# Kernel optimization log

Measured on AMD Instinct MI355X. Metric: run time of the kernel, lower is better.

The kernel has to match this reference:

```python
import jax, jax.numpy as jnp
import numpy as np

B, S, H = 2, 2048, 2048
NUM_HEADS, NUM_KV_HEADS, HEAD_DIM = 8, 1, 256
ROPE_THETA = 10000.0
NEG_INF = -1e9


def _rope_tables(seq_len, head_dim, base=ROPE_THETA):
    # cos/sin of shape [seq_len, head_dim], matching GemmaRotaryEmbedding
    inv_freq = 1.0 / (base ** (jnp.arange(0, head_dim, 2, dtype=jnp.float32) / head_dim))
    pos = jnp.arange(seq_len, dtype=jnp.float32)
    freqs = pos[:, None] * inv_freq[None, :]          # [S, D/2]
    emb = jnp.concatenate([freqs, freqs], axis=-1)    # [S, D]
    return jnp.cos(emb), jnp.sin(emb)


def _rotate_half(x):
    d = x.shape[-1] // 2
    return jnp.concatenate([-x[..., d:], x[..., :d]], axis=-1)


def setup_inputs() -> dict:
    key = jax.random.key(0)
    ks = jax.random.split(key, 5)
    hidden_states = jax.random.normal(ks[0], (B, S, H), dtype=jnp.float32)
    # additive causal mask: 0 where allowed, -inf above diagonal
    causal = jnp.tril(jnp.ones((S, S), dtype=bool))
    attention_mask = jnp.where(causal, 0.0, NEG_INF).astype(jnp.float32)[None, None]  # [1,1,S,S]
    sc = 1.0 / np.sqrt(H)
    Wq = jax.random.normal(ks[1], (H, NUM_HEADS * HEAD_DIM), dtype=jnp.float32) * sc
    Wk = jax.random.normal(ks[2], (H, NUM_KV_HEADS * HEAD_DIM), dtype=jnp.float32) * sc
    Wv = jax.random.normal(ks[3], (H, NUM_KV_HEADS * HEAD_DIM), dtype=jnp.float32) * sc
    Wo = jax.random.normal(ks[4], (NUM_HEADS * HEAD_DIM, H), dtype=jnp.float32) * sc
    return {"hidden_states": hidden_states, "attention_mask": attention_mask,
            "Wq": Wq, "Wk": Wk, "Wv": Wv, "Wo": Wo}


def reference(hidden_states, attention_mask, Wq, Wk, Wv, Wo):
    b, s, _ = hidden_states.shape
    g = NUM_HEADS // NUM_KV_HEADS  # query heads per kv head

    q = (hidden_states @ Wq).reshape(b, s, NUM_HEADS, HEAD_DIM).transpose(0, 2, 1, 3)      # [b,h,s,d]
    k = (hidden_states @ Wk).reshape(b, s, NUM_KV_HEADS, HEAD_DIM).transpose(0, 2, 1, 3)   # [b,kh,s,d]
    v = (hidden_states @ Wv).reshape(b, s, NUM_KV_HEADS, HEAD_DIM).transpose(0, 2, 1, 3)   # [b,kh,s,d]

    cos, sin = _rope_tables(s, HEAD_DIM)  # [s,d]
    cos = cos[None, None]                 # [1,1,s,d]
    sin = sin[None, None]
    q = q * cos + _rotate_half(q) * sin
    k = k * cos + _rotate_half(k) * sin

    # GQA attention without materializing repeated K/V: group query heads per kv head
    qg = q.reshape(b, NUM_KV_HEADS, g, s, HEAD_DIM)                       # [b,kh,g,s,d]
    scale = 1.0 / np.sqrt(HEAD_DIM)
    scores = jnp.einsum('bkgsd,bktd->bkgst', qg, k) * scale               # [b,kh,g,s,t]
    scores = scores + attention_mask[:, :, None]                          # broadcast [1,1,1,s,t]
    probs = jax.nn.softmax(scores, axis=-1)
    out = jnp.einsum('bkgst,bktd->bkgsd', probs, v)                       # [b,kh,g,s,d]
    out = out.reshape(b, NUM_HEADS, s, HEAD_DIM).transpose(0, 2, 1, 3).reshape(b, s, NUM_HEADS * HEAD_DIM)
    return out @ Wo
```

## Files before the change

kernel.cpp:

```cpp
#include <hip/hip_runtime.h>
#include <hip/hip_bf16.h>

typedef unsigned short u16;
typedef short short8 __attribute__((ext_vector_type(8)));
typedef float f32x4 __attribute__((ext_vector_type(4)));
typedef float f32x16 __attribute__((ext_vector_type(16)));
typedef u16 u16x4 __attribute__((ext_vector_type(4)));

__device__ __forceinline__ u16 f2bf(float f) {
    unsigned int u = __float_as_uint(f);
    u += 0x7fffu + ((u >> 16) & 1u);
    return (u16)(u >> 16);
}
__device__ __forceinline__ float bf2f(u16 s) {
    return __uint_as_float(((unsigned int)s) << 16);
}
__device__ __forceinline__ unsigned pack2(float lo, float hi) {
    union { __hip_bfloat162 h; unsigned u; } cv;
    cv.h = __float22bfloat162_rn(make_float2(lo, hi));
    return cv.u;
}
__device__ __forceinline__ f32x4 mfma16(short8 a, short8 b, f32x4 c) {
    return __builtin_amdgcn_mfma_f32_16x16x32_bf16(a, b, c, 0, 0, 0);
}
__device__ __forceinline__ f32x16 mfma32(short8 a, short8 b, f32x16 c) {
    return __builtin_amdgcn_mfma_f32_32x32x16_bf16(a, b, c, 0, 0, 0);
}
__device__ __forceinline__ void gld16(const void* g, void* l) {
    __builtin_amdgcn_global_load_lds(
        (const __attribute__((address_space(1))) unsigned int*)g,
        (__attribute__((address_space(3))) unsigned int*)l, 16, 0, 0);
}

#define BATCH 2
#define SEQ   2048
#define HID   2048
#define NH    8
#define HD    256
#define MROWS (BATCH * SEQ)

__global__ void k_cvt(const float* __restrict__ src, u16* __restrict__ dst, int n) {
    int i = (blockIdx.x * 256 + threadIdx.x) * 4;
    if (i >= n) return;
    float4 v = *(const float4*)(src + i);
    u16x4 o; o.x = f2bf(v.x); o.y = f2bf(v.y); o.z = f2bf(v.z); o.w = f2bf(v.w);
    *(u16x4*)(dst + i) = o;
}

__global__ __launch_bounds__(256) void k_wtall(const float* __restrict__ Wq,
                                               const float* __restrict__ Wk,
                                               const float* __restrict__ Wv,
                                               const float* __restrict__ Wo,
                                               u16* __restrict__ Wqkvt,
                                               u16* __restrict__ Wot) {
    const int cx = blockIdx.x;
    const float* W; u16* Wt; int N, n0;
    if (cx < 32)      { W = Wq; Wt = Wqkvt;                          N = 2048; n0 = cx << 6; }
    else if (cx < 36) { W = Wk; Wt = Wqkvt + (size_t)2048 * 2048;    N = 256;  n0 = (cx - 32) << 6; }
    else if (cx < 40) { W = Wv; Wt = Wqkvt + (size_t)2304 * 2048;    N = 256;  n0 = (cx - 36) << 6; }
    else              { W = Wo; Wt = Wot;                            N = 2048; n0 = (cx - 40) << 6; }

    __shared__ float tile[64][65];
    const int k0 = blockIdx.y << 6;
    const int tr = threadIdx.x >> 6, tc = threadIdx.x & 63;
#pragma unroll
    for (int i = 0; i < 16; i++)
        tile[i * 4 + tr][tc] = W[(size_t)(k0 + i * 4 + tr) * N + n0 + tc];
    __syncthreads();
#pragma unroll
    for (int i = 0; i < 16; i++) {
        int r = i * 4 + tr;
        Wt[(size_t)(n0 + r) * 2048 + k0 + tc] = f2bf(tile[tc][r]);
    }
}

__global__ __launch_bounds__(256) void k_vt(const u16* __restrict__ KVb, char* __restrict__ VS) {
    __shared__ u16 sT[64][72];
    const int bid = blockIdx.x;
    const int b = bid >> 7, kvt = (bid >> 2) & 31, dc = bid & 3;
    const int tr = threadIdx.x >> 6, tc = threadIdx.x & 63;
#pragma unroll
    for (int i = 0; i < 16; i++) {
        int kv = i * 4 + tr;
        sT[kv][tc] = KVb[((size_t)(b * SEQ + kvt * 64 + kv) << 9) + 256 + (dc << 6) + tc];
    }
    __syncthreads();
    char* obase = VS + ((size_t)b << 20) + (size_t)kvt * 32768;
#pragma unroll
    for (int e = 0; e < 2; e++) {
        int u = threadIdx.x * 2 + e;
        int dl = u >> 3, kvc = u & 7;
        union { u16 h[8]; uint4 q; } pk;
#pragma unroll
        for (int j = 0; j < 8; j++) pk.h[j] = sT[kvc * 8 + j][dl];
        int byte = dl * 512 + ((((dc << 7) + (kvc << 4))) ^ ((dl & 31) << 4));
        *(uint4*)(obase + byte) = pk.q;
    }
}

template<int FUSEQKV>
__global__ __launch_bounds__(256) void k_gemm(const u16* __restrict__ A,
                                              const u16* __restrict__ Bt,
                                              u16* __restrict__ Cq,
                                              u16* __restrict__ Ckv,
                                              float* __restrict__ Cf,
                                              int K, int nbx) {
    const int cpx = gridDim.x >> 3;
    const int t8  = (blockIdx.x & 7) * cpx + (blockIdx.x >> 3);
    const int m0 = (t8 / nbx) << 7;
    const int n0 = (t8 % nbx) << 7;

    const int tid = threadIdx.x, lane = tid & 63, wave = tid >> 6;
    const int g = lane >> 4, c = lane & 15;
    const int wrow = (wave >> 1) << 6, wcol = (wave & 1) << 6;

    __shared__ __align__(16) u16 sA[128 * 64];
    __shared__ __align__(16) u16 sB[128 * 64];

    const int srow = lane >> 3;
    const int scol = ((lane & 7) ^ srow) << 3;
    const u16* gA = A  + (size_t)(m0 + wave * 32 + srow) * K + scol;
    const u16* gB = Bt + (size_t)(n0 + wave * 32 + srow) * K + scol;
    u16* const lA = sA + wave * 32 * 64;
    u16* const lB = sB + wave * 32 * 64;

    f32x4 acc[4][4] = {};

    for (int k0 = 0; k0 < K; k0 += 64) {
        __syncthreads();
#pragma unroll
        for (int i = 0; i < 4; i++) {
            gld16(gA + k0 + (size_t)i * 8 * K, lA + i * 8 * 64);
            gld16(gB + k0 + (size_t)i * 8 * K, lB + i * 8 * 64);
        }
        __syncthreads();
#pragma unroll
        for (int ks = 0; ks < 2; ks++) {
            short8 aF[4], bF[4];
#pragma unroll
            for (int tt = 0; tt < 4; tt++) {
                const int ar = wrow + tt * 16 + c;
                const int br = wcol + tt * 16 + c;
                const int coff = ks * 64 + g * 16;
                aF[tt] = *(const short8*)((const char*)sA + ar * 128 + (coff ^ ((ar & 7) << 4)));
                bF[tt] = *(const short8*)((const char*)sB + br * 128 + (coff ^ ((br & 7) << 4)));
            }
#pragma unroll
            for (int mt = 0; mt < 4; mt++)
#pragma unroll
                for (int ntc = 0; ntc < 4; ntc++)
                    acc[mt][ntc] = mfma16(aF[mt], bF[ntc], acc[mt][ntc]);
        }
    }

#pragma unroll
    for (int mt = 0; mt < 4; mt++)
#pragma unroll
        for (int ntc = 0; ntc < 4; ntc++)
#pragma unroll
            for (int r = 0; r < 4; r++) {
                int row = m0 + wrow + mt * 16 + g * 4 + r;
                int col = n0 + wcol + ntc * 16 + c;
                float v = acc[mt][ntc][r];
                if (FUSEQKV) {
                    if (col < 2048) Cq [(size_t)row * 2048 + col] = f2bf(v);
                    else            Ckv[(size_t)row * 512 + (col - 2048)] = f2bf(v);
                } else {
                    Cf[(size_t)row * 2048 + col] = v;
                }
            }
}

__global__ void k_rope(u16* __restrict__ Qb, const u16* __restrict__ KVb,
                       char* __restrict__ KS) {
    int idx = blockIdx.x * 256 + threadIdx.x;
    const int QG = MROWS * NH * 16;
    if (idx < QG) {
        int row  = idx >> 7;
        int rest = idx & 127;
        int h = rest >> 4, d0 = (rest & 15) << 3;
        u16* base = Qb + (size_t)row * HID + h * HD + d0;
        int pos = row & (SEQ - 1);
        short8 lo = *(const short8*)(base);
        short8 hi = *(const short8*)(base + 128);
        short8 olo, ohi;
#pragma unroll
        for (int j = 0; j < 8; j++) {
            int d = d0 + j;
            float invf = __expf(-(float)d * (9.2103403719761836f / 128.0f));
            float ang = (float)pos * invf;
            float sn, cs; __sincosf(ang, &sn, &cs);
            float x0 = bf2f((u16)lo[j]);
            float x1 = bf2f((u16)hi[j]);
            olo[j] = (short)f2bf(x0 * cs - x1 * sn);
            ohi[j] = (short)f2bf(x1 * cs + x0 * sn);
        }
        *(short8*)(base)       = olo;
        *(short8*)(base + 128) = ohi;
    } else {
        int j0 = idx - QG;
        int row = j0 >> 4, d0 = (j0 & 15) << 3;
        const u16* src = KVb + (size_t)row * 512 + d0;
        int pos = row & (SEQ - 1);
        short8 lo = *(const short8*)(src);
        short8 hi = *(const short8*)(src + 128);
        short8 olo, ohi;
#pragma unroll
        for (int j = 0; j < 8; j++) {
            int d = d0 + j;
            float invf = __expf(-(float)d * (9.2103403719761836f / 128.0f));
            float ang = (float)pos * invf;
            float sn, cs; __sincosf(ang, &sn, &cs);
            float x0 = bf2f((u16)lo[j]);
            float x1 = bf2f((u16)hi[j]);
            olo[j] = (short)f2bf(x0 * cs - x1 * sn);
            ohi[j] = (short)f2bf(x1 * cs + x0 * sn);
        }
        int bb = row >> 11, sr = row & 2047;
        char* obase = KS + ((size_t)bb << 20) + (size_t)(sr >> 6) * 32768 + (sr & 63) * 512;
        int xr = (sr & 31) << 4;
        *(short8*)(obase + (((d0 << 1))       ^ xr)) = olo;
        *(short8*)(obase + (((d0 << 1) + 256) ^ xr)) = ohi;
    }
}

__global__ __launch_bounds__(256, 2) void k_attn(const u16* __restrict__ Q,
                                                 const char* __restrict__ KS,
                                                 const char* __restrict__ VS,
                                                 u16* __restrict__ Oa) {
    const int tid  = threadIdx.x;
    const int lane = tid & 63;
    const int wave = tid >> 6;
    const int l31  = lane & 31;
    const int hv   = lane >> 5;

    const int bid   = blockIdx.x;
    const int bh    = bid & 15;
    const int qpair = (bid >> 4) & 15;
    const int qidx  = (bid >> 8) ? (31 - qpair) : qpair;
    const int qb    = qidx << 6;
    const int b = bh >> 3, head = bh & 7;

    __shared__ __align__(16) char smem[66560];
    char*  const pK  = smem;
    char*  const pV  = smem + 32768;
    float* const sML = (float*)(smem + 65536);

    const int qg = qb + ((wave >> 1) << 5) + l31;
    short8 qf[16];
    {
        const u16* qptr = Q + (size_t)(b * SEQ + qg) * HID + head * HD + (hv << 3);
#pragma unroll
        for (int ks = 0; ks < 16; ks++)
            qf[ks] = *(const short8*)(qptr + (ks << 4));
    }

    f32x16 o[8] = {};
    float m = -1e30f, l = 0.f;

    const char* kgb = KS + ((size_t)b << 20);
    const char* vgb = VS + ((size_t)b << 20);
    const int   kxor  = l31 << 4;
    const char* kbase = pK + (((wave & 1) << 5) + l31) * 512;

    const int nt = qidx + 1;
    for (int t = 0; t < nt; t++) {
        __syncthreads();
#pragma unroll
        for (int i = 0; i < 8; i++) {
            int chunk = (i << 2) + wave;
            gld16(kgb + (size_t)t * 32768 + chunk * 1024 + lane * 16, pK + chunk * 1024);
            gld16(vgb + (size_t)t * 32768 + chunk * 1024 + lane * 16, pV + chunk * 1024);
        }
        __syncthreads();

        f32x16 sv0 = {}, sv1 = {};
#pragma unroll
        for (int ks = 0; ks < 16; ks += 2) {
            short8 kf0 = *(const short8*)(kbase + (((ks << 5) + (hv << 4)) ^ kxor));
            short8 kf1 = *(const short8*)(kbase + ((((ks + 1) << 5) + (hv << 4)) ^ kxor));
            sv0 = mfma32(kf0, qf[ks], sv0);
            sv1 = mfma32(kf1, qf[ks + 1], sv1);
        }
        f32x16 s = sv0 + sv1;

        float v[16];
        float mx = -3.0e38f;
        const bool diag = (t == nt - 1);
#pragma unroll
        for (int r = 0; r < 16; r++) {
            float x = s[r] * 0.0625f;
            if (diag) {
                int kvg = (t << 6) + ((wave & 1) << 5) + (r & 3) + ((r >> 2) << 3) + (hv << 2);
                if (kvg > qg) x = -3.0e38f;
            }
            v[r] = x;
            mx = fmaxf(mx, x);
        }
        mx = fmaxf(mx, __shfl_xor(mx, 32));
        if (!__all(mx <= m + 8.0f)) {
            float mn = fmaxf(m, mx);
            float sc = __expf(m - mn);
            l *= sc;
#pragma unroll
            for (int r = 0; r < 16; r++) {
                float scr = __shfl(sc, (r & 3) + ((r >> 2) << 3) + (hv << 2));
#pragma unroll
                for (int dt = 0; dt < 8; dt++) o[dt][r] *= scr;
            }
            m = mn;
        }
        float rs = 0.f;
#pragma unroll
        for (int r = 0; r < 16; r++) { v[r] = __expf(v[r] - m); rs += v[r]; }
        rs += __shfl_xor(rs, 32);
        l += rs;

        unsigned wd[8], pw[8];
#pragma unroll
        for (int i = 0; i < 8; i++) wd[i] = pack2(v[2 * i], v[2 * i + 1]);
#pragma unroll
        for (int i = 0; i < 8; i++) pw[i] = (unsigned)__shfl_xor((int)wd[i], 32);

#pragma unroll
        for (int ks2 = 0; ks2 < 2; ks2++) {
            union { unsigned u[4]; short8 s8; } fr;
            const int o4 = ks2 << 2;
            fr.u[0] = hv ? pw[o4 + 2] : wd[o4 + 0];
            fr.u[1] = hv ? pw[o4 + 3] : wd[o4 + 1];
            fr.u[2] = hv ? wd[o4 + 2] : pw[o4 + 0];
            fr.u[3] = hv ? wd[o4 + 3] : pw[o4 + 1];
            const int vcol = ((wave & 1) << 6) + (ks2 << 5) + (hv << 4);
#pragma unroll
            for (int dt = 0; dt < 8; dt++) {
                int row  = ((dt & 1) << 5) + l31;
                int colb = ((dt >> 1) << 7) + vcol;
                short8 vf = *(const short8*)(pV + row * 512 + (colb ^ kxor));
                o[dt] = mfma32(fr.s8, vf, o[dt]);
            }
        }
    }

    __syncthreads();
    if (lane < 32) {
        sML[(wave << 6) + (l31 << 1)]     = m;
        sML[(wave << 6) + (l31 << 1) + 1] = l;
    }
    __syncthreads();
    float m1 = sML[((wave ^ 1) << 6) + (l31 << 1)];
    float l1 = sML[((wave ^ 1) << 6) + (l31 << 1) + 1];
    float M  = fmaxf(m, m1);
    float e0 = __expf(m - M), e1 = __expf(m1 - M);
    float fac = e0 / (l * e0 + l1 * e1);
    float facr[16];
#pragma unroll
    for (int r = 0; r < 16; r++)
        facr[r] = __shfl(fac, (r & 3) + ((r >> 2) << 3) + (hv << 2));
#pragma unroll
    for (int dt = 0; dt < 8; dt++)
#pragma unroll
        for (int r = 0; r < 16; r++) o[dt][r] *= facr[r];

    float* sO = (float*)smem;
    if (wave & 1) {
#pragma unroll
        for (int dt = 0; dt < 8; dt++)
#pragma unroll
            for (int r = 0; r < 16; r++) {
                int q = (r & 3) + ((r >> 2) << 3) + (hv << 2);
                sO[((wave >> 1) << 13) + (q << 8) + (dt << 5) + l31] = o[dt][r];
            }
    }
    __syncthreads();
    if (!(wave & 1)) {
#pragma unroll
        for (int dt = 0; dt < 8; dt++)
#pragma unroll
            for (int r = 0; r < 16; r++) {
                int q = (r & 3) + ((r >> 2) << 3) + (hv << 2);
                float val = o[dt][r] + sO[((wave >> 1) << 13) + (q << 8) + (dt << 5) + l31];
                Oa[(size_t)(b * SEQ + qb + ((wave >> 1) << 5) + q) * HID
                   + head * HD + (dt << 5) + l31] = f2bf(val);
            }
    }
}

extern "C" void kernel_launch(void* const* d_in, const int* in_sizes, int n_in,
                              void* d_out, int out_size, void* d_ws, size_t ws_size,
                              hipStream_t stream) {
    const float* hidden = (const float*)d_in[0];
    const float* Wq = (const float*)d_in[2];
    const float* Wk = (const float*)d_in[3];
    const float* Wv = (const float*)d_in[4];
    const float* Wo = (const float*)d_in[5];
    float* out = (float*)d_out;

    char* ws = (char*)d_ws;
    u16* hid_bf = (u16*)(ws);
    u16* Wqkvt  = (u16*)(ws + (16u << 20));
    u16* Wot    = (u16*)(ws + (26u << 20));
    u16* Qb     = (u16*)(ws + (34u << 20));
    u16* KVb    = (u16*)(ws + (50u << 20));
    u16* Ab     = (u16*)(ws + (54u << 20));
    char* KS    = ws;
    char* VS    = ws + (2u << 20);

    k_cvt  <<<8192, 256, 0, stream>>>(hidden, hid_bf, MROWS * HID);
    k_wtall<<<dim3(72, 32), 256, 0, stream>>>(Wq, Wk, Wv, Wo, Wqkvt, Wot);

    k_gemm<1><<<640, 256, 0, stream>>>(hid_bf, Wqkvt, Qb, KVb, nullptr, 2048, 20);

    k_rope<<<2304, 256, 0, stream>>>(Qb, KVb, KS);
    k_vt  <<<256, 256, 0, stream>>>(KVb, VS);

    k_attn<<<512, 256, 0, stream>>>(Qb, KS, VS, Ab);

    k_gemm<0><<<512, 256, 0, stream>>>(Ab, Wot, nullptr, nullptr, out, 2048, 16);
}
```

Baseline: 223.1 us.

## Merge prep and post kernels; register-prefetch next K/V tile in attention

```diff
diff --git a/kernel.cpp b/kernel.cpp
--- a/kernel.cpp
+++ b/kernel.cpp
@@ -39,29 +39,31 @@
 #define HD    256
 #define MROWS (BATCH * SEQ)
 
-__global__ void k_cvt(const float* __restrict__ src, u16* __restrict__ dst, int n) {
-    int i = (blockIdx.x * 256 + threadIdx.x) * 4;
-    if (i >= n) return;
-    float4 v = *(const float4*)(src + i);
-    u16x4 o; o.x = f2bf(v.x); o.y = f2bf(v.y); o.z = f2bf(v.z); o.w = f2bf(v.w);
-    *(u16x4*)(dst + i) = o;
-}
-
-__global__ __launch_bounds__(256) void k_wtall(const float* __restrict__ Wq,
-                                               const float* __restrict__ Wk,
-                                               const float* __restrict__ Wv,
-                                               const float* __restrict__ Wo,
-                                               u16* __restrict__ Wqkvt,
-                                               u16* __restrict__ Wot) {
-    const int cx = blockIdx.x;
+__global__ __launch_bounds__(256) void k_prep(const float* __restrict__ hidden,
+                                              u16* __restrict__ hid_bf,
+                                              const float* __restrict__ Wq,
+                                              const float* __restrict__ Wk,
+                                              const float* __restrict__ Wv,
+                                              const float* __restrict__ Wo,
+                                              u16* __restrict__ Wqkvt,
+                                              u16* __restrict__ Wot) {
+    __shared__ float tile[64][65];
+    const int bx = blockIdx.x;
+    if (bx < 8192) {
+        int i = (bx * 256 + threadIdx.x) * 4;
+        float4 v = *(const float4*)(hidden + i);
+        u16x4 o; o.x = f2bf(v.x); o.y = f2bf(v.y); o.z = f2bf(v.z); o.w = f2bf(v.w);
+        *(u16x4*)(hid_bf + i) = o;
+        return;
+    }
+    const int idx = bx - 8192;
+    const int cx = idx % 72, ky = idx / 72;
     const float* W; u16* Wt; int N, n0;
-    if (cx < 32)      { W = Wq; Wt = Wqkvt;                          N = 2048; n0 = cx << 6; }
-    else if (cx < 36) { W = Wk; Wt = Wqkvt + (size_t)2048 * 2048;    N = 256;  n0 = (cx - 32) << 6; }
-    else if (cx < 40) { W = Wv; Wt = Wqkvt + (size_t)2304 * 2048;    N = 256;  n0 = (cx - 36) << 6; }
-    else              { W = Wo; Wt = Wot;                            N = 2048; n0 = (cx - 40) << 6; }
-
-    __shared__ float tile[64][65];
-    const int k0 = blockIdx.y << 6;
+    if (cx < 32)      { W = Wq; Wt = Wqkvt;                       N = 2048; n0 = cx << 6; }
+    else if (cx < 36) { W = Wk; Wt = Wqkvt + (size_t)2048 * 2048; N = 256;  n0 = (cx - 32) << 6; }
+    else if (cx < 40) { W = Wv; Wt = Wqkvt + (size_t)2304 * 2048; N = 256;  n0 = (cx - 36) << 6; }
+    else              { W = Wo; Wt = Wot;                         N = 2048; n0 = (cx - 40) << 6; }
+    const int k0 = ky << 6;
     const int tr = threadIdx.x >> 6, tc = threadIdx.x & 63;
 #pragma unroll
     for (int i = 0; i < 16; i++)
@@ -71,30 +73,6 @@
     for (int i = 0; i < 16; i++) {
         int r = i * 4 + tr;
         Wt[(size_t)(n0 + r) * 2048 + k0 + tc] = f2bf(tile[tc][r]);
-    }
-}
-
-__global__ __launch_bounds__(256) void k_vt(const u16* __restrict__ KVb, char* __restrict__ VS) {
-    __shared__ u16 sT[64][72];
-    const int bid = blockIdx.x;
-    const int b = bid >> 7, kvt = (bid >> 2) & 31, dc = bid & 3;
-    const int tr = threadIdx.x >> 6, tc = threadIdx.x & 63;
-#pragma unroll
-    for (int i = 0; i < 16; i++) {
-        int kv = i * 4 + tr;
-        sT[kv][tc] = KVb[((size_t)(b * SEQ + kvt * 64 + kv) << 9) + 256 + (dc << 6) + tc];
-    }
-    __syncthreads();
-    char* obase = VS + ((size_t)b << 20) + (size_t)kvt * 32768;
-#pragma unroll
-    for (int e = 0; e < 2; e++) {
-        int u = threadIdx.x * 2 + e;
-        int dl = u >> 3, kvc = u & 7;
-        union { u16 h[8]; uint4 q; } pk;
-#pragma unroll
-        for (int j = 0; j < 8; j++) pk.h[j] = sT[kvc * 8 + j][dl];
-        int byte = dl * 512 + ((((dc << 7) + (kvc << 4))) ^ ((dl & 31) << 4));
-        *(uint4*)(obase + byte) = pk.q;
     }
 }
 
@@ -171,56 +149,83 @@
             }
 }
 
-__global__ void k_rope(u16* __restrict__ Qb, const u16* __restrict__ KVb,
-                       char* __restrict__ KS) {
-    int idx = blockIdx.x * 256 + threadIdx.x;
-    const int QG = MROWS * NH * 16;
-    if (idx < QG) {
-        int row  = idx >> 7;
-        int rest = idx & 127;
-        int h = rest >> 4, d0 = (rest & 15) << 3;
-        u16* base = Qb + (size_t)row * HID + h * HD + d0;
-        int pos = row & (SEQ - 1);
-        short8 lo = *(const short8*)(base);
-        short8 hi = *(const short8*)(base + 128);
-        short8 olo, ohi;
-#pragma unroll
-        for (int j = 0; j < 8; j++) {
-            int d = d0 + j;
-            float invf = __expf(-(float)d * (9.2103403719761836f / 128.0f));
-            float ang = (float)pos * invf;
-            float sn, cs; __sincosf(ang, &sn, &cs);
-            float x0 = bf2f((u16)lo[j]);
-            float x1 = bf2f((u16)hi[j]);
-            olo[j] = (short)f2bf(x0 * cs - x1 * sn);
-            ohi[j] = (short)f2bf(x1 * cs + x0 * sn);
-        }
-        *(short8*)(base)       = olo;
-        *(short8*)(base + 128) = ohi;
-    } else {
-        int j0 = idx - QG;
-        int row = j0 >> 4, d0 = (j0 & 15) << 3;
-        const u16* src = KVb + (size_t)row * 512 + d0;
-        int pos = row & (SEQ - 1);
-        short8 lo = *(const short8*)(src);
-        short8 hi = *(const short8*)(src + 128);
-        short8 olo, ohi;
-#pragma unroll
-        for (int j = 0; j < 8; j++) {
-            int d = d0 + j;
-            float invf = __expf(-(float)d * (9.2103403719761836f / 128.0f));
-            float ang = (float)pos * invf;
-            float sn, cs; __sincosf(ang, &sn, &cs);
-            float x0 = bf2f((u16)lo[j]);
-            float x1 = bf2f((u16)hi[j]);
-            olo[j] = (short)f2bf(x0 * cs - x1 * sn);
-            ohi[j] = (short)f2bf(x1 * cs + x0 * sn);
-        }
-        int bb = row >> 11, sr = row & 2047;
-        char* obase = KS + ((size_t)bb << 20) + (size_t)(sr >> 6) * 32768 + (sr & 63) * 512;
-        int xr = (sr & 31) << 4;
-        *(short8*)(obase + (((d0 << 1))       ^ xr)) = olo;
-        *(short8*)(obase + (((d0 << 1) + 256) ^ xr)) = ohi;
+__global__ __launch_bounds__(256) void k_post(u16* __restrict__ Qb,
+                                              const u16* __restrict__ KVb,
+                                              char* __restrict__ KS,
+                                              char* __restrict__ VS) {
+    __shared__ u16 sT[64][72];
+    const int bx = blockIdx.x;
+    if (bx < 2304) {
+        int idx = bx * 256 + threadIdx.x;
+        const int QG = MROWS * NH * 16;
+        if (idx < QG) {
+            int row  = idx >> 7;
+            int rest = idx & 127;
+            int h = rest >> 4, d0 = (rest & 15) << 3;
+            u16* base = Qb + (size_t)row * HID + h * HD + d0;
+            int pos = row & (SEQ - 1);
+            short8 lo = *(const short8*)(base);
+            short8 hi = *(const short8*)(base + 128);
+            short8 olo, ohi;
+#pragma unroll
+            for (int j = 0; j < 8; j++) {
+                int d = d0 + j;
+                float invf = __expf(-(float)d * (9.2103403719761836f / 128.0f));
+                float ang = (float)pos * invf;
+                float sn, cs; __sincosf(ang, &sn, &cs);
+                float x0 = bf2f((u16)lo[j]);
+                float x1 = bf2f((u16)hi[j]);
+                olo[j] = (short)f2bf(x0 * cs - x1 * sn);
+                ohi[j] = (short)f2bf(x1 * cs + x0 * sn);
+            }
+            *(short8*)(base)       = olo;
+            *(short8*)(base + 128) = ohi;
+        } else {
+            int j0 = idx - QG;
+            int row = j0 >> 4, d0 = (j0 & 15) << 3;
+            const u16* src = KVb + (size_t)row * 512 + d0;
+            int pos = row & (SEQ - 1);
+            short8 lo = *(const short8*)(src);
+            short8 hi = *(const short8*)(src + 128);
+            short8 olo, ohi;
+#pragma unroll
+            for (int j = 0; j < 8; j++) {
+                int d = d0 + j;
+                float invf = __expf(-(float)d * (9.2103403719761836f / 128.0f));
+                float ang = (float)pos * invf;
+                float sn, cs; __sincosf(ang, &sn, &cs);
+                float x0 = bf2f((u16)lo[j]);
+                float x1 = bf2f((u16)hi[j]);
+                olo[j] = (short)f2bf(x0 * cs - x1 * sn);
+                ohi[j] = (short)f2bf(x1 * cs + x0 * sn);
+            }
+            int bb = row >> 11, sr = row & 2047;
+            char* obase = KS + ((size_t)bb << 20) + (size_t)(sr >> 6) * 32768 + (sr & 63) * 512;
+            int xr = (sr & 31) << 4;
+            *(short8*)(obase + (((d0 << 1))       ^ xr)) = olo;
+            *(short8*)(obase + (((d0 << 1) + 256) ^ xr)) = ohi;
+        }
+        return;
+    }
+    const int bid = bx - 2304;
+    const int b = bid >> 7, kvt = (bid >> 2) & 31, dc = bid & 3;
+    const int tr = threadIdx.x >> 6, tc = threadIdx.x & 63;
+#pragma unroll
+    for (int i = 0; i < 16; i++) {
+        int kv = i * 4 + tr;
+        sT[kv][tc] = KVb[((size_t)(b * SEQ + kvt * 64 + kv) << 9) + 256 + (dc << 6) + tc];
+    }
+    __syncthreads();
+    char* obase = VS + ((size_t)b << 20) + (size_t)kvt * 32768;
+#pragma unroll
+    for (int e = 0; e < 2; e++) {
+        int u = threadIdx.x * 2 + e;
+        int dl = u >> 3, kvc = u & 7;
+        union { u16 h[8]; uint4 q; } pk;
+#pragma unroll
+        for (int j = 0; j < 8; j++) pk.h[j] = sT[kvc * 8 + j][dl];
+        int byte = dl * 512 + ((((dc << 7) + (kvc << 4))) ^ ((dl & 31) << 4));
+        *(uint4*)(obase + byte) = pk.q;
     }
 }
 
@@ -264,15 +269,31 @@
     const char* kbase = pK + (((wave & 1) << 5) + l31) * 512;
 
     const int nt = qidx + 1;
+    short8 kv8[8], vv8[8];
+#pragma unroll
+    for (int i = 0; i < 8; i++) {
+        int ch = (i << 2) + wave;
+        kv8[i] = *(const short8*)(kgb + ch * 1024 + lane * 16);
+        vv8[i] = *(const short8*)(vgb + ch * 1024 + lane * 16);
+    }
+
     for (int t = 0; t < nt; t++) {
         __syncthreads();
 #pragma unroll
         for (int i = 0; i < 8; i++) {
-            int chunk = (i << 2) + wave;
-            gld16(kgb + (size_t)t * 32768 + chunk * 1024 + lane * 16, pK + chunk * 1024);
-            gld16(vgb + (size_t)t * 32768 + chunk * 1024 + lane * 16, pV + chunk * 1024);
+            int ch = (i << 2) + wave;
+            *(short8*)(pK + ch * 1024 + lane * 16) = kv8[i];
+            *(short8*)(pV + ch * 1024 + lane * 16) = vv8[i];
         }
         __syncthreads();
+        if (t + 1 < nt) {
+#pragma unroll
+            for (int i = 0; i < 8; i++) {
+                int ch = (i << 2) + wave;
+                kv8[i] = *(const short8*)(kgb + (size_t)(t + 1) * 32768 + ch * 1024 + lane * 16);
+                vv8[i] = *(const short8*)(vgb + (size_t)(t + 1) * 32768 + ch * 1024 + lane * 16);
+            }
+        }
 
         f32x16 sv0 = {}, sv1 = {};
 #pragma unroll
@@ -405,13 +426,11 @@
     char* KS    = ws;
     char* VS    = ws + (2u << 20);
 
-    k_cvt  <<<8192, 256, 0, stream>>>(hidden, hid_bf, MROWS * HID);
-    k_wtall<<<dim3(72, 32), 256, 0, stream>>>(Wq, Wk, Wv, Wo, Wqkvt, Wot);
+    k_prep<<<10496, 256, 0, stream>>>(hidden, hid_bf, Wq, Wk, Wv, Wo, Wqkvt, Wot);
 
     k_gemm<1><<<640, 256, 0, stream>>>(hid_bf, Wqkvt, Qb, KVb, nullptr, 2048, 20);
 
-    k_rope<<<2304, 256, 0, stream>>>(Qb, KVb, KS);
-    k_vt  <<<256, 256, 0, stream>>>(KVb, VS);
+    k_post<<<2560, 256, 0, stream>>>(Qb, KVb, KS, VS);
 
     k_attn<<<512, 256, 0, stream>>>(Qb, KS, VS, Ab);
 
```

After: 328.4 us. 1.47x slower.
